# Performance work log

Hardware: AMD Instinct MI355X
Metric: run time of the kernel (lower is better)

Reference implementation:

```python
import jax, jax.numpy as jnp
import numpy as np

B, SX, SY, D = 64, 512, 512, 1024


def setup_inputs() -> dict:
    key = jax.random.key(0)
    k1, k2, k3, k4 = jax.random.split(key, 4)
    x = jax.random.normal(k1, (B, SX, D), dtype=jnp.float32)
    y = jax.random.normal(k2, (B, SY, D), dtype=jnp.float32)
    # Keras 'uniform' init ~ U(-0.05, 0.05); scale kept small and realistic
    W = jax.random.uniform(k3, (D, D), dtype=jnp.float32, minval=-0.05, maxval=0.05)
    b = jax.random.uniform(k4, (D,), dtype=jnp.float32, minval=-0.05, maxval=0.05)
    return {"x": x, "y": y, "W": W, "b": b}


def reference(x, y, W, b):
    # proj: (x @ W + b) -> [B, Sx, D]
    proj = jnp.einsum('bsd,de->bse', x, W) + b
    # attention scores: proj @ y^T -> [B, Sx, Sy]
    att = jnp.einsum('bsd,btd->bst', proj, y)
    # row-wise stable softmax over last axis (matches manual max-subtract softmax)
    nor = jax.nn.softmax(att, axis=-1)
    # weighted sum over y -> [B, Sx, D]
    return jnp.einsum('bst,btd->bsd', nor, y)
```

## Files before the change

### kernel.cpp

```cpp
#include <hip/hip_runtime.h>


typedef float  f32x4  __attribute__((ext_vector_type(4)));
typedef _Float16 f16x8 __attribute__((ext_vector_type(8)));
typedef _Float16 f16x4 __attribute__((ext_vector_type(4)));
typedef __bf16 bf16x8 __attribute__((ext_vector_type(8)));
typedef __bf16 bf16x4 __attribute__((ext_vector_type(4)));

#define MFMA_F16(a, b, c)  __builtin_amdgcn_mfma_f32_16x16x32_f16((a), (b), (c), 0, 0, 0)
#define MFMA_BF16(a, b, c) __builtin_amdgcn_mfma_f32_16x16x32_bf16((a), (b), (c), 0, 0, 0)

#define WAIT_VM(N)  do { asm volatile("s_waitcnt vmcnt(" #N ")" ::: "memory"); \
                         __builtin_amdgcn_sched_barrier(0); } while (0)

__device__ __forceinline__ void async16(const void* g, void* lds) {
    __builtin_amdgcn_global_load_lds(
        (const __attribute__((address_space(1))) unsigned int*)g,
        (__attribute__((address_space(3))) unsigned int*)lds, 16, 0, 0);
}

template <bool DOW>
__global__ void prep_all_kernel(const float* __restrict__ y, _Float16* __restrict__ yf,
                                _Float16* __restrict__ yT, const float* __restrict__ x,
                                f16x4* __restrict__ xh, f16x4* __restrict__ xl,
                                const float* __restrict__ W, _Float16* __restrict__ WT)
{
    __shared__ _Float16 LT[64][72];
    const int tid = threadIdx.x;
    const int bid = blockIdx.x;

    if (bid < 8192) {
        const int b   = bid >> 7;
        const int rem = bid & 127;
        const int sy0 = (rem >> 4) * 64;
        const int d0  = (rem & 15) * 64;
        const int r0 = tid >> 4;
        const int c4 = (tid & 15) * 4;
        #pragma unroll
        for (int i = 0; i < 4; ++i) {
            const int r = r0 + i * 16;
            const float4 v = *(const float4*)&y[((size_t)b * 512 + sy0 + r) * 1024 + d0 + c4];
            const f16x4 hv = {(_Float16)v.x, (_Float16)v.y, (_Float16)v.z, (_Float16)v.w};
            *(f16x4*)&yf[((size_t)b * 512 + sy0 + r) * 1024 + d0 + c4] = hv;
            #pragma unroll
            for (int cc = 0; cc < 4; ++cc) {
                const int c = (cc + (tid & 3)) & 3;
                LT[c4 + c][r] = hv[c];
            }
        }
        __syncthreads();
        #pragma unroll
        for (int i = 0; i < 4; ++i) {
            const int dr = r0 + i * 16;
            const f16x4 v = *(const f16x4*)&LT[dr][(tid & 15) * 4];
            *(f16x4*)&yT[((size_t)b * 1024 + d0 + dr) * 512 + sy0 + (tid & 15) * 4] = v;
        }
    } else if (bid < 10240) {
        int i = (bid - 8192) * 256 + tid;
        const float4* in = (const float4*)x;
        for (; i < 8388608; i += 2048 * 256) {
            const float4 v = in[i];
            const _Float16 h0 = (_Float16)v.x, h1 = (_Float16)v.y,
                           h2 = (_Float16)v.z, h3 = (_Float16)v.w;
            xh[i] = (f16x4){h0, h1, h2, h3};
            xl[i] = (f16x4){(_Float16)(v.x - (float)h0), (_Float16)(v.y - (float)h1),
                            (_Float16)(v.z - (float)h2), (_Float16)(v.w - (float)h3)};
        }
    } else if constexpr (DOW) {
        const int rem = bid - 10240;
        const int k0 = (rem >> 4) * 64;
        const int n0 = (rem & 15) * 64;
        const int r0 = tid >> 4;
        const int c4 = (tid & 15) * 4;
        #pragma unroll
        for (int i = 0; i < 4; ++i) {
            const int r = r0 + i * 16;
            const float4 v = *(const float4*)&W[(size_t)(k0 + r) * 1024 + n0 + c4];
            const f16x4 hv = {(_Float16)v.x, (_Float16)v.y, (_Float16)v.z, (_Float16)v.w};
            #pragma unroll
            for (int cc = 0; cc < 4; ++cc) {
                const int c = (cc + (tid & 3)) & 3;
                LT[c4 + c][r] = hv[c];
            }
        }
        __syncthreads();
        #pragma unroll
        for (int i = 0; i < 4; ++i) {
            const int dr = r0 + i * 16;
            const f16x4 v = *(const f16x4*)&LT[dr][(tid & 15) * 4];
            *(f16x4*)&WT[(size_t)(n0 + dr) * 1024 + k0 + (tid & 15) * 4] = v;
        }
    }
}

template <bool PRE>
__global__ __launch_bounds__(256, 2)
void proj_f16_kernel(const _Float16* __restrict__ xh, const _Float16* __restrict__ xl,
                     const _Float16* __restrict__ WT, const float* __restrict__ W,
                     const float* __restrict__ bias, char* __restrict__ outc)
{
    __shared__ __align__(16) char psm[73728];

    const int tid = threadIdx.x, lane = tid & 63, wave = tid >> 6;
    const int swz = (blockIdx.x & 7) * 256 + (blockIdx.x >> 3);
    const int m0 = (swz >> 3) * 128, n0 = (swz & 7) * 128;
    const int wm = (wave >> 1) * 64, wn = (wave & 1) * 64;
    const int ar = lane & 15;
    const int qs  = ((lane >> 4) ^ ((lane >> 1) & 3)) * 8;
    const int gcS = ((lane & 3) ^ ((lane >> 3) & 3)) * 8;
    const int lrow = lane >> 2;
    const int wkb = tid & 7;
    const int wn4 = (tid >> 3) * 4;

    f32x4 acc[4][4];
    #pragma unroll
    for (int i = 0; i < 4; ++i)
        #pragma unroll
        for (int j = 0; j < 4; ++j)
            acc[i][j] = (f32x4){0.f, 0.f, 0.f, 0.f};

    auto STAGE = [&](int t, int bi) {
        const int k0 = t * 32;
        _Float16 (*Xh)[32] = (_Float16(*)[32])(psm + bi * 24576);
        _Float16 (*Xl)[32] = (_Float16(*)[32])(psm + bi * 24576 + 8192);
        _Float16 (*Wf)[32] = (_Float16(*)[32])(psm + bi * 24576 + 16384);
        #pragma unroll
        for (int tt = 0; tt < 2; ++tt) {
            const int r = wave * 32 + tt * 16 + lrow;
            async16(&xh[(size_t)(m0 + r) * 1024 + k0 + gcS], &Xh[wave * 32 + tt * 16][0]);
            async16(&xl[(size_t)(m0 + r) * 1024 + k0 + gcS], &Xl[wave * 32 + tt * 16][0]);
            if constexpr (PRE)
                async16(&WT[(size_t)(n0 + r) * 1024 + k0 + gcS], &Wf[wave * 32 + tt * 16][0]);
        }
        if constexpr (!PRE) {
            const size_t wb = (size_t)(k0 + wkb * 4) * 1024 + n0 + wn4;
            const float4 v0 = *(const float4*)&W[wb];
            const float4 v1 = *(const float4*)&W[wb + 1024];
            const float4 v2 = *(const float4*)&W[wb + 2048];
            const float4 v3 = *(const float4*)&W[wb + 3072];
            const float rv[4][4] = {{v0.x, v0.y, v0.z, v0.w},
                                    {v1.x, v1.y, v1.z, v1.w},
                                    {v2.x, v2.y, v2.z, v2.w},
                                    {v3.x, v3.y, v3.z, v3.w}};
            #pragma unroll
            for (int j = 0; j < 4; ++j) {
                const int R = wn4 + j;
                const f16x4 hv = {(_Float16)rv[0][j], (_Float16)rv[1][j],
                                  (_Float16)rv[2][j], (_Float16)rv[3][j]};
                const int c = (wkb >> 1) ^ ((R >> 1) & 3);
                *(f16x4*)&Wf[R][c * 8 + (wkb & 1) * 4] = hv;
            }
        }
    };

    STAGE(0, 0);
    STAGE(1, 1);
    STAGE(2, 2);

    int bi = 0;
    for (int t = 0; t < 32; ++t) {
        if (t < 30)       { if constexpr (PRE) WAIT_VM(12); else WAIT_VM(8); }
        else if (t == 30) { if constexpr (PRE) WAIT_VM(6);  else WAIT_VM(4); }
        else              { WAIT_VM(0); }
        __builtin_amdgcn_s_barrier();

        _Float16 (*Xh)[32] = (_Float16(*)[32])(psm + bi * 24576);
        _Float16 (*Xl)[32] = (_Float16(*)[32])(psm + bi * 24576 + 8192);
        _Float16 (*Wf)[32] = (_Float16(*)[32])(psm + bi * 24576 + 16384);
        f16x8 ah[4], al[4], bfv[4];
        #pragma unroll
        for (int f = 0; f < 4; ++f) {
            ah[f]  = *(const f16x8*)&Xh[wm + f * 16 + ar][qs];
            al[f]  = *(const f16x8*)&Xl[wm + f * 16 + ar][qs];
            bfv[f] = *(const f16x8*)&Wf[wn + f * 16 + ar][qs];
        }
        #pragma unroll
        for (int i = 0; i < 4; ++i)
            #pragma unroll
            for (int j = 0; j < 4; ++j) {
                acc[i][j] = MFMA_F16(ah[i], bfv[j], acc[i][j]);
                acc[i][j] = MFMA_F16(al[i], bfv[j], acc[i][j]);
            }
        __builtin_amdgcn_s_barrier();

        if (t < 29) {
            STAGE(t + 3, bi);
            if constexpr (!PRE)
                asm volatile("s_waitcnt lgkmcnt(0)" ::: "memory");
        }
        bi = (bi == 2) ? 0 : bi + 1;
    }

    _Float16* Ep = (_Float16*)psm;
    const int q4 = (lane >> 4) * 4;
    #pragma unroll
    for (int j = 0; j < 4; ++j) {
        const int nloc = wn + j * 16 + ar;
        const float bv = bias[n0 + nloc];
        const int nidx = (nloc >> 3) * 16 + (nloc & 7);
        #pragma unroll
        for (int i = 0; i < 4; ++i)
            #pragma unroll
            for (int r = 0; r < 4; ++r) {
                const int Rl = wm + i * 16 + q4 + r;
                const float v = acc[i][j][r] + bv;
                const _Float16 h = (_Float16)v;
                Ep[Rl * 256 + nidx]     = h;
                Ep[Rl * 256 + nidx + 8] = (_Float16)(v - (float)h);
            }
    }
    __syncthreads();
    #pragma unroll
    for (int c = 0; c < 16; ++c) {
        const int lin = c * 4096 + tid * 16;
        const int row = lin >> 9;
        const int off = lin & 511;
        *(float4*)(outc + (size_t)(m0 + row) * 4096 + n0 * 4 + off)
            = *(const float4*)(psm + lin);
    }
}

__global__ __launch_bounds__(256, 2)
void attn_f16_kernel(const _Float16* __restrict__ yf, const _Float16* __restrict__ yT,
                     char* __restrict__ outc)
{
    __shared__ _Float16 Pbuf[64][520];
    __shared__ float    Red[512];

    const int tid = threadIdx.x, lane = tid & 63, wave = tid >> 6;
    const int swzb = (blockIdx.x & 7) * 64 + (blockIdx.x >> 3);
    const int b = swzb >> 3, sx0 = (swzb & 7) * 64;
    const int pbase = b * 512 + sx0;
    const int ar = lane & 15, q = lane >> 4, qk = q * 8;
    const size_t ybase = (size_t)b * 512 * 1024;

    f32x4 s2[4][8];
    #pragma unroll
    for (int ri = 0; ri < 4; ++ri)
        #pragma unroll
        for (int t = 0; t < 8; ++t)
            s2[ri][t] = (f32x4){0.f, 0.f, 0.f, 0.f};

    const char* aptr = outc + (size_t)(pbase + ar) * 4096;
    const _Float16* yw = yf + ybase + (size_t)(wave * 128 + ar) * 1024;

    f16x8 A0H[4], A0L[4], A1H[4], A1L[4];
    auto LOADA = [&](int kk, f16x8 (&AH)[4], f16x8 (&AL)[4]) {
        #pragma unroll
        for (int ri = 0; ri < 4; ++ri) {
            const char* p = aptr + (size_t)ri * 65536 + (size_t)(kk * 4 + q) * 32;
            AH[ri] = *(const f16x8*)p;
            AL[ri] = *(const f16x8*)(p + 16);
        }
    };

    LOADA(0, A0H, A0L);
    LOADA(1, A1H, A1L);

    for (int kk = 0; kk < 32; kk += 2) {
        {
            f16x8 bf[8];
            #pragma unroll
            for (int t = 0; t < 8; ++t)
                bf[t] = *(const f16x8*)&yw[(size_t)t * 16384 + kk * 32 + qk];
            #pragma unroll
            for (int ri = 0; ri < 4; ++ri)
                #pragma unroll
                for (int t = 0; t < 8; ++t) {
                    s2[ri][t] = MFMA_F16(A0H[ri], bf[t], s2[ri][t]);
                    s2[ri][t] = MFMA_F16(A0L[ri], bf[t], s2[ri][t]);
                }
            if (kk + 2 < 32) LOADA(kk + 2, A0H, A0L);
        }
        {
            f16x8 bf[8];
            #pragma unroll
            for (int t = 0; t < 8; ++t)
                bf[t] = *(const f16x8*)&yw[(size_t)t * 16384 + (kk + 1) * 32 + qk];
            #pragma unroll
            for (int ri = 0; ri < 4; ++ri)
                #pragma unroll
                for (int t = 0; t < 8; ++t) {
                    s2[ri][t] = MFMA_F16(A1H[ri], bf[t], s2[ri][t]);
                    s2[ri][t] = MFMA_F16(A1L[ri], bf[t], s2[ri][t]);
                }
            if (kk + 3 < 32) LOADA(kk + 3, A1H, A1L);
        }
    }

    float pm[4][4];
    #pragma unroll
    for (int ri = 0; ri < 4; ++ri)
        #pragma unroll
        for (int r = 0; r < 4; ++r) {
            float m = -3.0e38f;
            #pragma unroll
            for (int t = 0; t < 8; ++t) m = fmaxf(m, s2[ri][t][r]);
            pm[ri][r] = m;
        }
    #pragma unroll
    for (int off = 1; off < 16; off <<= 1)
        #pragma unroll
        for (int ri = 0; ri < 4; ++ri)
            #pragma unroll
            for (int r = 0; r < 4; ++r)
                pm[ri][r] = fmaxf(pm[ri][r], __shfl_xor(pm[ri][r], off, 64));
    if (ar == 0) {
        #pragma unroll
        for (int ri = 0; ri < 4; ++ri)
            #pragma unroll
            for (int r = 0; r < 4; ++r)
                Red[wave * 64 + ri * 16 + q * 4 + r] = pm[ri][r];
    }
    __syncthreads();
    float gm[4][4];
    #pragma unroll
    for (int ri = 0; ri < 4; ++ri)
        #pragma unroll
        for (int r = 0; r < 4; ++r) {
            const int row = ri * 16 + q * 4 + r;
            gm[ri][r] = fmaxf(fmaxf(Red[row], Red[64 + row]),
                              fmaxf(Red[128 + row], Red[192 + row]));
        }
    float ps[4][4];
    #pragma unroll
    for (int ri = 0; ri < 4; ++ri)
        #pragma unroll
        for (int r = 0; r < 4; ++r) {
            float sum = 0.f;
            #pragma unroll
            for (int t = 0; t < 8; ++t) {
                const float e = __expf(s2[ri][t][r] - gm[ri][r]);
                s2[ri][t][r] = e;
                sum += e;
            }
            ps[ri][r] = sum;
        }
    #pragma unroll
    for (int off = 1; off < 16; off <<= 1)
        #pragma unroll
        for (int ri = 0; ri < 4; ++ri)
            #pragma unroll
            for (int r = 0; r < 4; ++r)
                ps[ri][r] += __shfl_xor(ps[ri][r], off, 64);
    if (ar == 0) {
        #pragma unroll
        for (int ri = 0; ri < 4; ++ri)
            #pragma unroll
            for (int r = 0; r < 4; ++r)
                Red[256 + wave * 64 + ri * 16 + q * 4 + r] = ps[ri][r];
    }
    __syncthreads();
    float inv[4][4];
    #pragma unroll
    for (int ri = 0; ri < 4; ++ri)
        #pragma unroll
        for (int r = 0; r < 4; ++r) {
            const int row = 256 + ri * 16 + q * 4 + r;
            inv[ri][r] = 1.0f / (Red[row] + Red[64 + row] + Red[128 + row] + Red[192 + row]);
        }
    #pragma unroll
    for (int ri = 0; ri < 4; ++ri)
        #pragma unroll
        for (int t = 0; t < 8; ++t)
            #pragma unroll
            for (int r = 0; r < 4; ++r)
                Pbuf[ri * 16 + q * 4 + r][wave * 128 + t * 16 + ar]
                    = (_Float16)(s2[ri][t][r] * inv[ri][r]);
    __syncthreads();

    float* outF = (float*)outc;
    #pragma unroll
    for (int dc = 0; dc < 2; ++dc) {
        f32x4 o2[4][8];
        #pragma unroll
        for (int ri = 0; ri < 4; ++ri)
            #pragma unroll
            for (int t = 0; t < 8; ++t)
                o2[ri][t] = (f32x4){0.f, 0.f, 0.f, 0.f};

        const _Float16* ytw = yT + ((size_t)b * 1024 + wave * 256 + dc * 128 + ar) * 512;

        for (int kk = 0; kk < 16; ++kk) {
            f16x8 a2[4], b2[8];
            #pragma unroll
            for (int ri = 0; ri < 4; ++ri)
                a2[ri] = *(const f16x8*)&Pbuf[ri * 16 + ar][kk * 32 + qk];
            #pragma unroll
            for (int t = 0; t < 8; ++t)
                b2[t] = *(const f16x8*)&ytw[(size_t)t * 16 * 512 + kk * 32 + qk];
            #pragma unroll
            for (int ri = 0; ri < 4; ++ri)
                #pragma unroll
                for (int t = 0; t < 8; ++t)
                    o2[ri][t] = MFMA_F16(a2[ri], b2[t], o2[ri][t]);
        }
        #pragma unroll
        for (int ri = 0; ri < 4; ++ri)
            #pragma unroll
            for (int t = 0; t < 8; ++t)
                #pragma unroll
                for (int r = 0; r < 4; ++r)
                    outF[(size_t)(pbase + ri * 16 + q * 4 + r) * 1024
                         + wave * 256 + dc * 128 + t * 16 + ar] = o2[ri][t][r];
    }
}


__device__ __forceinline__ void cvt4(const float4 v, bf16x4& h, bf16x4& l) {
    const float f0 = v.x, f1 = v.y, f2 = v.z, f3 = v.w;
    const __bf16 h0 = (__bf16)f0, h1 = (__bf16)f1, h2 = (__bf16)f2, h3 = (__bf16)f3;
    h = (bf16x4){h0, h1, h2, h3};
    l = (bf16x4){(__bf16)(f0 - (float)h0), (__bf16)(f1 - (float)h1),
                 (__bf16)(f2 - (float)h2), (__bf16)(f3 - (float)h3)};
}

__global__ __launch_bounds__(256, 2)
void proj_kernel_fb(const float* __restrict__ x, const float* __restrict__ W,
                    const float* __restrict__ bias, float* __restrict__ proj)
{
    __shared__ __bf16 Ah[128][40];
    __shared__ __bf16 Al[128][40];
    __shared__ __bf16 Bh[128][40];
    __shared__ __bf16 Bl[128][40];

    const int tid = threadIdx.x, lane = tid & 63, wave = tid >> 6;
    const int wm = (wave >> 1) * 64, wn = (wave & 1) * 64;
    const int m0 = (blockIdx.x >> 3) * 128, n0 = (blockIdx.x & 7) * 128;
    const int ar = lane & 15, ak = (lane >> 4) * 8;

    f32x4 acc[4][4];
    #pragma unroll
    for (int i = 0; i < 4; ++i)
        #pragma unroll
        for (int j = 0; j < 4; ++j)
            acc[i][j] = (f32x4){0.f, 0.f, 0.f, 0.f};

    const int xr = tid >> 3, xc = (tid & 7) * 4;
    const int wkb = tid >> 5, wn4 = (tid & 31) * 4;

    for (int k0 = 0; k0 < 1024; k0 += 32) {
        __syncthreads();
        #pragma unroll
        for (int it = 0; it < 4; ++it) {
            const int r = xr + it * 32;
            const float4 v = *(const float4*)&x[(size_t)(m0 + r) * 1024 + k0 + xc];
            bf16x4 h, l; cvt4(v, h, l);
            *(bf16x4*)&Ah[r][xc] = h;
            *(bf16x4*)&Al[r][xc] = l;
        }
        {
            const size_t wb = (size_t)(k0 + wkb * 4) * 1024 + n0 + wn4;
            const float4 v0 = *(const float4*)&W[wb];
            const float4 v1 = *(const float4*)&W[wb + 1024];
            const float4 v2 = *(const float4*)&W[wb + 2048];
            const float4 v3 = *(const float4*)&W[wb + 3072];
            const float rv[4][4] = {{v0.x, v0.y, v0.z, v0.w},
                                    {v1.x, v1.y, v1.z, v1.w},
                                    {v2.x, v2.y, v2.z, v2.w},
                                    {v3.x, v3.y, v3.z, v3.w}};
            #pragma unroll
            for (int j = 0; j < 4; ++j) {
                bf16x4 h, l;
                #pragma unroll
                for (int kk = 0; kk < 4; ++kk) {
                    const float f = rv[kk][j];
                    const __bf16 hb = (__bf16)f;
                    h[kk] = hb;
                    l[kk] = (__bf16)(f - (float)hb);
                }
                *(bf16x4*)&Bh[wn4 + j][wkb * 4] = h;
                *(bf16x4*)&Bl[wn4 + j][wkb * 4] = l;
            }
        }
        __syncthreads();

        bf16x8 a_h[4], a_l[4], b_h[4], b_l[4];
        #pragma unroll
        for (int f = 0; f < 4; ++f) {
            a_h[f] = *(const bf16x8*)&Ah[wm + f * 16 + ar][ak];
            a_l[f] = *(const bf16x8*)&Al[wm + f * 16 + ar][ak];
            b_h[f] = *(const bf16x8*)&Bh[wn + f * 16 + ar][ak];
            b_l[f] = *(const bf16x8*)&Bl[wn + f * 16 + ar][ak];
        }
        #pragma unroll
        for (int i = 0; i < 4; ++i)
            #pragma unroll
            for (int j = 0; j < 4; ++j) {
                acc[i][j] = MFMA_BF16(a_h[i], b_h[j], acc[i][j]);
                acc[i][j] = MFMA_BF16(a_l[i], b_h[j], acc[i][j]);
                acc[i][j] = MFMA_BF16(a_h[i], b_l[j], acc[i][j]);
            }
    }

    const int q4 = (lane >> 4) * 4;
    #pragma unroll
    for (int j = 0; j < 4; ++j) {
        const int n = n0 + wn + j * 16 + ar;
        const float bv = bias[n];
        #pragma unroll
        for (int i = 0; i < 4; ++i) {
            const size_t base = (size_t)(m0 + wm + i * 16 + q4) * 1024 + n;
            #pragma unroll
            for (int r = 0; r < 4; ++r)
                proj[base + (size_t)r * 1024] = acc[i][j][r] + bv;
        }
    }
}

__global__ __launch_bounds__(256, 1)
void attn_kernel_fb(const float* __restrict__ y, float* __restrict__ out)
{
    __shared__ __bf16 Ph[64][40];
    __shared__ __bf16 Pl[64][40];
    __shared__ __bf16 Yh[128][40];
    __shared__ __bf16 Yl[128][40];
    __shared__ __bf16 Pbuf[64][520];

    const int tid = threadIdx.x, lane = tid & 63, wave = tid >> 6;
    const int b = blockIdx.x >> 3, sx0 = (blockIdx.x & 7) * 64;
    const size_t ybase = (size_t)b * 512 * 1024;
    const size_t pbase = ((size_t)b * 512 + sx0) * 1024;
    const int ar = lane & 15, ak = (lane >> 4) * 8, q = lane >> 4;

    f32x4 s[4][8];
    #pragma unroll
    for (int nb = 0; nb < 4; ++nb)
        #pragma unroll
        for (int f = 0; f < 8; ++f)
            s[nb][f] = (f32x4){0.f, 0.f, 0.f, 0.f};

    const int pr = tid >> 3, pc = (tid & 7) * 4;

    for (int k0 = 0; k0 < 1024; k0 += 32) {
        __syncthreads();
        #pragma unroll
        for (int it = 0; it < 2; ++it) {
            const int r = pr + it * 32;
            const float4 v = *(const float4*)&out[pbase + (size_t)r * 1024 + k0 + pc];
            bf16x4 h, l; cvt4(v, h, l);
            *(bf16x4*)&Ph[r][pc] = h;
            *(bf16x4*)&Pl[r][pc] = l;
        }
        #pragma unroll
        for (int nb = 0; nb < 4; ++nb) {
            if (nb) __syncthreads();
            const int sy0 = nb * 128;
            #pragma unroll
            for (int it = 0; it < 4; ++it) {
                const int r = pr + it * 32;
                const float4 v = *(const float4*)&y[ybase + (size_t)(sy0 + r) * 1024 + k0 + pc];
                bf16x4 h, l; cvt4(v, h, l);
                *(bf16x4*)&Yh[r][pc] = h;
                *(bf16x4*)&Yl[r][pc] = l;
            }
            __syncthreads();
            const bf16x8 a_h = *(const bf16x8*)&Ph[wave * 16 + ar][ak];
            const bf16x8 a_l = *(const bf16x8*)&Pl[wave * 16 + ar][ak];
            #pragma unroll
            for (int f = 0; f < 8; ++f) {
                const bf16x8 b_h = *(const bf16x8*)&Yh[f * 16 + ar][ak];
                const bf16x8 b_l = *(const bf16x8*)&Yl[f * 16 + ar][ak];
                s[nb][f] = MFMA_BF16(a_h, b_h, s[nb][f]);
                s[nb][f] = MFMA_BF16(a_l, b_h, s[nb][f]);
                s[nb][f] = MFMA_BF16(a_h, b_l, s[nb][f]);
            }
        }
    }

    #pragma unroll
    for (int r = 0; r < 4; ++r) {
        float m = -3.0e38f;
        #pragma unroll
        for (int nb = 0; nb < 4; ++nb)
            #pragma unroll
            for (int f = 0; f < 8; ++f)
                m = fmaxf(m, s[nb][f][r]);
        #pragma unroll
        for (int off = 1; off < 16; off <<= 1)
            m = fmaxf(m, __shfl_xor(m, off, 64));
        float sum = 0.f;
        #pragma unroll
        for (int nb = 0; nb < 4; ++nb)
            #pragma unroll
            for (int f = 0; f < 8; ++f) {
                const float e = __expf(s[nb][f][r] - m);
                s[nb][f][r] = e;
                sum += e;
            }
        #pragma unroll
        for (int off = 1; off < 16; off <<= 1)
            sum += __shfl_xor(sum, off, 64);
        const float inv = 1.0f / sum;
        #pragma unroll
        for (int nb = 0; nb < 4; ++nb)
            #pragma unroll
            for (int f = 0; f < 8; ++f)
                s[nb][f][r] *= inv;
    }
    #pragma unroll
    for (int nb = 0; nb < 4; ++nb)
        #pragma unroll
        for (int f = 0; f < 8; ++f)
            #pragma unroll
            for (int r = 0; r < 4; ++r)
                Pbuf[wave * 16 + q * 4 + r][nb * 128 + f * 16 + ar] = (__bf16)s[nb][f][r];

    const int y2kb = tid >> 5, y2n4 = (tid & 31) * 4;
    for (int d0 = 0; d0 < 1024; d0 += 128) {
        f32x4 o[8];
        #pragma unroll
        for (int f = 0; f < 8; ++f) o[f] = (f32x4){0.f, 0.f, 0.f, 0.f};

        for (int k0 = 0; k0 < 512; k0 += 32) {
            __syncthreads();
            const size_t yb = ybase + (size_t)(k0 + y2kb * 4) * 1024 + d0 + y2n4;
            const float4 v0 = *(const float4*)&y[yb];
            const float4 v1 = *(const float4*)&y[yb + 1024];
            const float4 v2 = *(const float4*)&y[yb + 2048];
            const float4 v3 = *(const float4*)&y[yb + 3072];
            const float rv[4][4] = {{v0.x, v0.y, v0.z, v0.w},
                                    {v1.x, v1.y, v1.z, v1.w},
                                    {v2.x, v2.y, v2.z, v2.w},
                                    {v3.x, v3.y, v3.z, v3.w}};
            #pragma unroll
            for (int j = 0; j < 4; ++j) {
                const bf16x4 h = (bf16x4){(__bf16)rv[0][j], (__bf16)rv[1][j],
                                          (__bf16)rv[2][j], (__bf16)rv[3][j]};
                *(bf16x4*)&Yh[y2n4 + j][y2kb * 4] = h;
            }
            __syncthreads();
            const bf16x8 a = *(const bf16x8*)&Pbuf[wave * 16 + ar][k0 + ak];
            #pragma unroll
            for (int f = 0; f < 8; ++f) {
                const bf16x8 bb = *(const bf16x8*)&Yh[f * 16 + ar][ak];
                o[f] = MFMA_BF16(a, bb, o[f]);
            }
        }
        #pragma unroll
        for (int f = 0; f < 8; ++f)
            #pragma unroll
            for (int r = 0; r < 4; ++r)
                out[pbase + (size_t)(wave * 16 + q * 4 + r) * 1024 + d0 + f * 16 + ar] = o[f][r];
    }
}


extern "C" void kernel_launch(void* const* d_in, const int* in_sizes, int n_in,
                              void* d_out, int out_size, void* d_ws, size_t ws_size,
                              hipStream_t stream) {
    (void)in_sizes; (void)n_in; (void)out_size;
    const float* x    = (const float*)d_in[0];
    const float* y    = (const float*)d_in[1];
    const float* W    = (const float*)d_in[2];
    const float* bias = (const float*)d_in[3];

    if (ws_size >= 268435456ULL) {
        _Float16* yf = (_Float16*)d_ws;
        _Float16* yT = yf + 33554432;
        _Float16* xh = yT + 33554432;
        _Float16* xl = xh + 33554432;
        _Float16* WT = xl + 33554432;
        const bool pre = ws_size >= 268435456ULL + 2097152ULL;

        if (pre) {
            prep_all_kernel<true><<<dim3(10496), dim3(256), 0, stream>>>(
                y, yf, yT, x, (f16x4*)xh, (f16x4*)xl, W, WT);
            proj_f16_kernel<true><<<dim3(2048), dim3(256), 0, stream>>>(xh, xl, WT, W, bias,
                                                                        (char*)d_out);
        } else {
            prep_all_kernel<false><<<dim3(10240), dim3(256), 0, stream>>>(
                y, yf, yT, x, (f16x4*)xh, (f16x4*)xl, W, nullptr);
            proj_f16_kernel<false><<<dim3(2048), dim3(256), 0, stream>>>(xh, xl, nullptr, W,
                                                                         bias, (char*)d_out);
        }
        attn_f16_kernel<<<dim3(512), dim3(256), 0, stream>>>(yf, yT, (char*)d_out);
    } else {
        float* out = (float*)d_out;
        proj_kernel_fb<<<dim3(256 * 8), dim3(256), 0, stream>>>(x, W, bias, out);
        attn_kernel_fb<<<dim3(64 * 8), dim3(256), 0, stream>>>(y, out);
    }
}
```

Before: 693.3 us.

## Stage y tiles through swizzled LDS with async loads in score GEMM

The first GEMM of the attention kernel used to read y fragments straight from global memory into registers. It now double-buffers y K-slices into LDS with global_load_lds async copies, using an XOR swizzle to avoid bank conflicts, and reuses the LDS region that later holds Pbuf. The MFMA order is also split so all high-part products issue before the low-part products. The aim is to overlap y fetches with MFMA work and cut global load latency, at the cost of manual vmcnt accounting. Each wave reads only its own rows, so no barrier is used, which could be a correctness risk.

```diff
diff --git a/kernel.cpp b/kernel.cpp
--- a/kernel.cpp
+++ b/kernel.cpp
@@ -224,14 +224,20 @@
 void attn_f16_kernel(const _Float16* __restrict__ yf, const _Float16* __restrict__ yT,
                      char* __restrict__ outc)
 {
-    __shared__ _Float16 Pbuf[64][520];
-    __shared__ float    Red[512];
+    __shared__ __align__(16) char smem[68608];
+    _Float16 (*Yb0)[32]   = (_Float16(*)[32])smem;
+    _Float16 (*Yb1)[32]   = (_Float16(*)[32])(smem + 32768);
+    _Float16 (*Pbuf)[520] = (_Float16(*)[520])smem;
+    float*    Red         = (float*)(smem + 66560);
 
     const int tid = threadIdx.x, lane = tid & 63, wave = tid >> 6;
     const int swzb = (blockIdx.x & 7) * 64 + (blockIdx.x >> 3);
     const int b = swzb >> 3, sx0 = (swzb & 7) * 64;
     const int pbase = b * 512 + sx0;
     const int ar = lane & 15, q = lane >> 4, qk = q * 8;
+    const int qs  = (q ^ ((lane >> 1) & 3)) * 8;
+    const int gcS = ((lane & 3) ^ ((lane >> 3) & 3)) * 8;
+    const int lrow = lane >> 2;
     const size_t ybase = (size_t)b * 512 * 1024;
 
     f32x4 s2[4][8];
@@ -242,8 +248,15 @@
             s2[ri][t] = (f32x4){0.f, 0.f, 0.f, 0.f};
 
     const char* aptr = outc + (size_t)(pbase + ar) * 4096;
-    const _Float16* yw = yf + ybase + (size_t)(wave * 128 + ar) * 1024;
-
+
+    auto STAGE0 = [&](int kk, _Float16 (*Yb)[32]) {
+        const int k0 = kk * 32;
+        #pragma unroll
+        for (int t = 0; t < 8; ++t) {
+            const int r = wave * 128 + t * 16 + lrow;
+            async16(&yf[ybase + (size_t)r * 1024 + k0 + gcS], &Yb[wave * 128 + t * 16][0]);
+        }
+    };
     f16x8 A0H[4], A0L[4], A1H[4], A1L[4];
     auto LOADA = [&](int kk, f16x8 (&AH)[4], f16x8 (&AL)[4]) {
         #pragma unroll
@@ -253,40 +266,42 @@
             AL[ri] = *(const f16x8*)(p + 16);
         }
     };
-
+    auto HALF = [&](int kk, f16x8 (&AH)[4], f16x8 (&AL)[4], _Float16 (*Yb)[32], bool more) {
+        f16x8 bf[8];
+        #pragma unroll
+        for (int t = 0; t < 8; ++t)
+            bf[t] = *(const f16x8*)&Yb[wave * 128 + t * 16 + ar][qs];
+        #pragma unroll
+        for (int ri = 0; ri < 4; ++ri)
+            #pragma unroll
+            for (int t = 0; t < 8; ++t)
+                s2[ri][t] = MFMA_F16(AH[ri], bf[t], s2[ri][t]);
+        #pragma unroll
+        for (int ri = 0; ri < 4; ++ri)
+            #pragma unroll
+            for (int t = 0; t < 8; ++t)
+                s2[ri][t] = MFMA_F16(AL[ri], bf[t], s2[ri][t]);
+        if (more) {
+            LOADA(kk + 2, AH, AL);
+            STAGE0(kk + 2, Yb);
+        }
+    };
+
+    STAGE0(0, Yb0);
     LOADA(0, A0H, A0L);
     LOADA(1, A1H, A1L);
-
-    for (int kk = 0; kk < 32; kk += 2) {
-        {
-            f16x8 bf[8];
-            #pragma unroll
-            for (int t = 0; t < 8; ++t)
-                bf[t] = *(const f16x8*)&yw[(size_t)t * 16384 + kk * 32 + qk];
-            #pragma unroll
-            for (int ri = 0; ri < 4; ++ri)
-                #pragma unroll
-                for (int t = 0; t < 8; ++t) {
-                    s2[ri][t] = MFMA_F16(A0H[ri], bf[t], s2[ri][t]);
-                    s2[ri][t] = MFMA_F16(A0L[ri], bf[t], s2[ri][t]);
-                }
-            if (kk + 2 < 32) LOADA(kk + 2, A0H, A0L);
-        }
-        {
-            f16x8 bf[8];
-            #pragma unroll
-            for (int t = 0; t < 8; ++t)
-                bf[t] = *(const f16x8*)&yw[(size_t)t * 16384 + (kk + 1) * 32 + qk];
-            #pragma unroll
-            for (int ri = 0; ri < 4; ++ri)
-                #pragma unroll
-                for (int t = 0; t < 8; ++t) {
-                    s2[ri][t] = MFMA_F16(A1H[ri], bf[t], s2[ri][t]);
-                    s2[ri][t] = MFMA_F16(A1L[ri], bf[t], s2[ri][t]);
-                }
-            if (kk + 3 < 32) LOADA(kk + 3, A1H, A1L);
-        }
-    }
+    STAGE0(1, Yb1);
+
+    for (int kk = 0; kk < 30; kk += 2) {
+        WAIT_VM(16);
+        HALF(kk, A0H, A0L, Yb0, true);
+        WAIT_VM(16);
+        HALF(kk + 1, A1H, A1L, Yb1, true);
+    }
+    WAIT_VM(16);
+    HALF(30, A0H, A0L, Yb0, false);
+    WAIT_VM(0);
+    HALF(31, A1H, A1L, Yb1, false);
 
     float pm[4][4];
     #pragma unroll
```

New measurement: 739.2 us. 1.07x slower.

## Split score computation into two column halves with online-softmax rescaling

Applied to the files above, without the earlier changes.

The attention kernel now computes the 64x512 score tile in two passes of 256 columns each. Each wave holds a 4x4 accumulator block instead of 4x8, which cuts register pressure. The B operand is now register double-buffered alongside A. Softmax is done flash-style: each half is exponentiated against its own running max, the first half in LDS is rescaled by exp(m1-m), and the 1/sum normalization is deferred to the output store. The cost is an extra pass over the first half of Pbuf, more reductions and barriers, and re-reading the A operand twice.

```diff
diff --git a/kernel.cpp b/kernel.cpp
--- a/kernel.cpp
+++ b/kernel.cpp
@@ -225,7 +225,7 @@
                      char* __restrict__ outc)
 {
     __shared__ _Float16 Pbuf[64][520];
-    __shared__ float    Red[512];
+    __shared__ float    Red[1024];
 
     const int tid = threadIdx.x, lane = tid & 63, wave = tid >> 6;
     const int swzb = (blockIdx.x & 7) * 64 + (blockIdx.x >> 3);
@@ -234,15 +234,7 @@
     const int ar = lane & 15, q = lane >> 4, qk = q * 8;
     const size_t ybase = (size_t)b * 512 * 1024;
 
-    f32x4 s2[4][8];
-    #pragma unroll
-    for (int ri = 0; ri < 4; ++ri)
-        #pragma unroll
-        for (int t = 0; t < 8; ++t)
-            s2[ri][t] = (f32x4){0.f, 0.f, 0.f, 0.f};
-
     const char* aptr = outc + (size_t)(pbase + ar) * 4096;
-    const _Float16* yw = yf + ybase + (size_t)(wave * 128 + ar) * 1024;
 
     f16x8 A0H[4], A0L[4], A1H[4], A1L[4];
     auto LOADA = [&](int kk, f16x8 (&AH)[4], f16x8 (&AL)[4]) {
@@ -253,120 +245,254 @@
             AL[ri] = *(const f16x8*)(p + 16);
         }
     };
-
-    LOADA(0, A0H, A0L);
-    LOADA(1, A1H, A1L);
-
-    for (int kk = 0; kk < 32; kk += 2) {
-        {
-            f16x8 bf[8];
-            #pragma unroll
-            for (int t = 0; t < 8; ++t)
-                bf[t] = *(const f16x8*)&yw[(size_t)t * 16384 + kk * 32 + qk];
-            #pragma unroll
-            for (int ri = 0; ri < 4; ++ri)
-                #pragma unroll
-                for (int t = 0; t < 8; ++t) {
-                    s2[ri][t] = MFMA_F16(A0H[ri], bf[t], s2[ri][t]);
-                    s2[ri][t] = MFMA_F16(A0L[ri], bf[t], s2[ri][t]);
+    f16x8 B0[4], B1[4];
+    auto LOADB = [&](int cb, int kk, f16x8 (&Bv)[4]) {
+        #pragma unroll
+        for (int t = 0; t < 4; ++t)
+            Bv[t] = *(const f16x8*)&yf[ybase + (size_t)(cb + t * 16 + ar) * 1024
+                                       + kk * 32 + qk];
+    };
+
+    f32x4 s2[4][4];
+    float mp1[4][4];
+    float inv_[4][4];
+
+    {
+        const int cb = wave * 64;
+        #pragma unroll
+        for (int ri = 0; ri < 4; ++ri)
+            #pragma unroll
+            for (int t = 0; t < 4; ++t)
+                s2[ri][t] = (f32x4){0.f, 0.f, 0.f, 0.f};
+        LOADA(0, A0H, A0L);
+        LOADA(1, A1H, A1L);
+        LOADB(cb, 0, B0);
+        LOADB(cb, 1, B1);
+        for (int kk = 0; kk < 32; kk += 2) {
+            #pragma unroll
+            for (int ri = 0; ri < 4; ++ri)
+                #pragma unroll
+                for (int t = 0; t < 4; ++t) {
+                    s2[ri][t] = MFMA_F16(A0H[ri], B0[t], s2[ri][t]);
+                    s2[ri][t] = MFMA_F16(A0L[ri], B0[t], s2[ri][t]);
                 }
-            if (kk + 2 < 32) LOADA(kk + 2, A0H, A0L);
-        }
-        {
-            f16x8 bf[8];
-            #pragma unroll
-            for (int t = 0; t < 8; ++t)
-                bf[t] = *(const f16x8*)&yw[(size_t)t * 16384 + (kk + 1) * 32 + qk];
-            #pragma unroll
-            for (int ri = 0; ri < 4; ++ri)
-                #pragma unroll
-                for (int t = 0; t < 8; ++t) {
-                    s2[ri][t] = MFMA_F16(A1H[ri], bf[t], s2[ri][t]);
-                    s2[ri][t] = MFMA_F16(A1L[ri], bf[t], s2[ri][t]);
+            if (kk + 2 < 32) { LOADA(kk + 2, A0H, A0L); LOADB(cb, kk + 2, B0); }
+            #pragma unroll
+            for (int ri = 0; ri < 4; ++ri)
+                #pragma unroll
+                for (int t = 0; t < 4; ++t) {
+                    s2[ri][t] = MFMA_F16(A1H[ri], B1[t], s2[ri][t]);
+                    s2[ri][t] = MFMA_F16(A1L[ri], B1[t], s2[ri][t]);
                 }
-            if (kk + 3 < 32) LOADA(kk + 3, A1H, A1L);
-        }
-    }
-
-    float pm[4][4];
-    #pragma unroll
-    for (int ri = 0; ri < 4; ++ri)
-        #pragma unroll
-        for (int r = 0; r < 4; ++r) {
-            float m = -3.0e38f;
-            #pragma unroll
-            for (int t = 0; t < 8; ++t) m = fmaxf(m, s2[ri][t][r]);
-            pm[ri][r] = m;
-        }
-    #pragma unroll
-    for (int off = 1; off < 16; off <<= 1)
-        #pragma unroll
-        for (int ri = 0; ri < 4; ++ri)
-            #pragma unroll
-            for (int r = 0; r < 4; ++r)
-                pm[ri][r] = fmaxf(pm[ri][r], __shfl_xor(pm[ri][r], off, 64));
-    if (ar == 0) {
-        #pragma unroll
-        for (int ri = 0; ri < 4; ++ri)
-            #pragma unroll
-            for (int r = 0; r < 4; ++r)
-                Red[wave * 64 + ri * 16 + q * 4 + r] = pm[ri][r];
-    }
-    __syncthreads();
-    float gm[4][4];
+            if (kk + 3 < 32) { LOADA(kk + 3, A1H, A1L); LOADB(cb, kk + 3, B1); }
+        }
+        float pm[4][4];
+        #pragma unroll
+        for (int ri = 0; ri < 4; ++ri)
+            #pragma unroll
+            for (int r = 0; r < 4; ++r) {
+                float m = -3.0e38f;
+                #pragma unroll
+                for (int t = 0; t < 4; ++t) m = fmaxf(m, s2[ri][t][r]);
+                pm[ri][r] = m;
+            }
+        #pragma unroll
+        for (int off = 1; off < 16; off <<= 1)
+            #pragma unroll
+            for (int ri = 0; ri < 4; ++ri)
+                #pragma unroll
+                for (int r = 0; r < 4; ++r)
+                    pm[ri][r] = fmaxf(pm[ri][r], __shfl_xor(pm[ri][r], off, 64));
+        if (ar == 0) {
+            #pragma unroll
+            for (int ri = 0; ri < 4; ++ri)
+                #pragma unroll
+                for (int r = 0; r < 4; ++r)
+                    Red[wave * 64 + ri * 16 + q * 4 + r] = pm[ri][r];
+        }
+        __syncthreads();
+        #pragma unroll
+        for (int ri = 0; ri < 4; ++ri)
+            #pragma unroll
+            for (int r = 0; r < 4; ++r) {
+                const int row = ri * 16 + q * 4 + r;
+                mp1[ri][r] = fmaxf(fmaxf(Red[row], Red[64 + row]),
+                                   fmaxf(Red[128 + row], Red[192 + row]));
+            }
+        if (wave == 0 && ar == 0) {
+            #pragma unroll
+            for (int ri = 0; ri < 4; ++ri)
+                #pragma unroll
+                for (int r = 0; r < 4; ++r)
+                    Red[512 + ri * 16 + q * 4 + r] = mp1[ri][r];
+        }
+        float ps[4][4];
+        #pragma unroll
+        for (int ri = 0; ri < 4; ++ri)
+            #pragma unroll
+            for (int r = 0; r < 4; ++r) {
+                float sum = 0.f;
+                #pragma unroll
+                for (int t = 0; t < 4; ++t) {
+                    const float e = __expf(s2[ri][t][r] - mp1[ri][r]);
+                    s2[ri][t][r] = e;
+                    sum += e;
+                }
+                ps[ri][r] = sum;
+            }
+        #pragma unroll
+        for (int off = 1; off < 16; off <<= 1)
+            #pragma unroll
+            for (int ri = 0; ri < 4; ++ri)
+                #pragma unroll
+                for (int r = 0; r < 4; ++r)
+                    ps[ri][r] += __shfl_xor(ps[ri][r], off, 64);
+        if (ar == 0) {
+            #pragma unroll
+            for (int ri = 0; ri < 4; ++ri)
+                #pragma unroll
+                for (int r = 0; r < 4; ++r)
+                    Red[256 + wave * 64 + ri * 16 + q * 4 + r] = ps[ri][r];
+        }
+        #pragma unroll
+        for (int ri = 0; ri < 4; ++ri)
+            #pragma unroll
+            for (int t = 0; t < 4; ++t)
+                #pragma unroll
+                for (int r = 0; r < 4; ++r)
+                    Pbuf[ri * 16 + q * 4 + r][cb + t * 16 + ar]
+                        = (_Float16)s2[ri][t][r];
+        __syncthreads();
+    }
+
+    {
+        const int cb = 256 + wave * 64;
+        #pragma unroll
+        for (int ri = 0; ri < 4; ++ri)
+            #pragma unroll
+            for (int t = 0; t < 4; ++t)
+                s2[ri][t] = (f32x4){0.f, 0.f, 0.f, 0.f};
+        LOADA(0, A0H, A0L);
+        LOADA(1, A1H, A1L);
+        LOADB(cb, 0, B0);
+        LOADB(cb, 1, B1);
+        for (int kk = 0; kk < 32; kk += 2) {
+            #pragma unroll
+            for (int ri = 0; ri < 4; ++ri)
+                #pragma unroll
+                for (int t = 0; t < 4; ++t) {
+                    s2[ri][t] = MFMA_F16(A0H[ri], B0[t], s2[ri][t]);
+                    s2[ri][t] = MFMA_F16(A0L[ri], B0[t], s2[ri][t]);
+                }
+            if (kk + 2 < 32) { LOADA(kk + 2, A0H, A0L); LOADB(cb, kk + 2, B0); }
+            #pragma unroll
+            for (int ri = 0; ri < 4; ++ri)
+                #pragma unroll
+                for (int t = 0; t < 4; ++t) {
+                    s2[ri][t] = MFMA_F16(A1H[ri], B1[t], s2[ri][t]);
+                    s2[ri][t] = MFMA_F16(A1L[ri], B1[t], s2[ri][t]);
+                }
+            if (kk + 3 < 32) { LOADA(kk + 3, A1H, A1L); LOADB(cb, kk + 3, B1); }
+        }
+        float pm[4][4];
+        #pragma unroll
+        for (int ri = 0; ri < 4; ++ri)
+            #pragma unroll
+            for (int r = 0; r < 4; ++r) {
+                float m = -3.0e38f;
+                #pragma unroll
+                for (int t = 0; t < 4; ++t) m = fmaxf(m, s2[ri][t][r]);
+                pm[ri][r] = m;
+            }
+        #pragma unroll
+        for (int off = 1; off < 16; off <<= 1)
+            #pragma unroll
+            for (int ri = 0; ri < 4; ++ri)
+                #pragma unroll
+                for (int r = 0; r < 4; ++r)
+                    pm[ri][r] = fmaxf(pm[ri][r], __shfl_xor(pm[ri][r], off, 64));
+        if (ar == 0) {
+            #pragma unroll
+            for (int ri = 0; ri < 4; ++ri)
+                #pragma unroll
+                for (int r = 0; r < 4; ++r)
+                    Red[wave * 64 + ri * 16 + q * 4 + r] = pm[ri][r];
+        }
+        __syncthreads();
+        float ps[4][4];
+        #pragma unroll
+        for (int ri = 0; ri < 4; ++ri)
+            #pragma unroll
+            for (int r = 0; r < 4; ++r) {
+                const int row = ri * 16 + q * 4 + r;
+                const float m2 = fmaxf(fmaxf(Red[row], Red[64 + row]),
+                                       fmaxf(Red[128 + row], Red[192 + row]));
+                const float m = fmaxf(mp1[ri][r], m2);
+                float sum = 0.f;
+                #pragma unroll
+                for (int t = 0; t < 4; ++t) {
+                    const float e = __expf(s2[ri][t][r] - m);
+                    s2[ri][t][r] = e;
+                    sum += e;
+                }
+                ps[ri][r] = sum;
+            }
+        #pragma unroll
+        for (int off = 1; off < 16; off <<= 1)
+            #pragma unroll
+            for (int ri = 0; ri < 4; ++ri)
+                #pragma unroll
+                for (int r = 0; r < 4; ++r)
+                    ps[ri][r] += __shfl_xor(ps[ri][r], off, 64);
+        if (ar == 0) {
+            #pragma unroll
+            for (int ri = 0; ri < 4; ++ri)
+                #pragma unroll
+                for (int r = 0; r < 4; ++r)
+                    Red[576 + wave * 64 + ri * 16 + q * 4 + r] = ps[ri][r];
+        }
+        #pragma unroll
+        for (int ri = 0; ri < 4; ++ri)
+            #pragma unroll
+            for (int t = 0; t < 4; ++t)
+                #pragma unroll
+                for (int r = 0; r < 4; ++r)
+                    Pbuf[ri * 16 + q * 4 + r][cb + t * 16 + ar]
+                        = (_Float16)s2[ri][t][r];
+        __syncthreads();
+    }
+
+    {
+        const int srow = tid >> 2;
+        const int c0 = (tid & 3) * 64;
+        const float m1r = Red[512 + srow];
+        const float m2r = fmaxf(fmaxf(Red[srow], Red[64 + srow]),
+                                fmaxf(Red[128 + srow], Red[192 + srow]));
+        const float a1 = __expf(m1r - fmaxf(m1r, m2r));
+        #pragma unroll
+        for (int cs = 0; cs < 8; ++cs) {
+            f16x8 v = *(f16x8*)&Pbuf[srow][c0 + cs * 8];
+            #pragma unroll
+            for (int e = 0; e < 8; ++e)
+                v[e] = (_Float16)((float)v[e] * a1);
+            *(f16x8*)&Pbuf[srow][c0 + cs * 8] = v;
+        }
+    }
     #pragma unroll
     for (int ri = 0; ri < 4; ++ri)
         #pragma unroll
         for (int r = 0; r < 4; ++r) {
             const int row = ri * 16 + q * 4 + r;
-            gm[ri][r] = fmaxf(fmaxf(Red[row], Red[64 + row]),
-                              fmaxf(Red[128 + row], Red[192 + row]));
-        }
-    float ps[4][4];
-    #pragma unroll
-    for (int ri = 0; ri < 4; ++ri)
-        #pragma unroll
-        for (int r = 0; r < 4; ++r) {
-            float sum = 0.f;
-            #pragma unroll
-            for (int t = 0; t < 8; ++t) {
-                const float e = __expf(s2[ri][t][r] - gm[ri][r]);
-                s2[ri][t][r] = e;
-                sum += e;
-            }
-            ps[ri][r] = sum;
-        }
-    #pragma unroll
-    for (int off = 1; off < 16; off <<= 1)
-        #pragma unroll
-        for (int ri = 0; ri < 4; ++ri)
-            #pragma unroll
-            for (int r = 0; r < 4; ++r)
-                ps[ri][r] += __shfl_xor(ps[ri][r], off, 64);
-    if (ar == 0) {
-        #pragma unroll
-        for (int ri = 0; ri < 4; ++ri)
-            #pragma unroll
-            for (int r = 0; r < 4; ++r)
-                Red[256 + wave * 64 + ri * 16 + q * 4 + r] = ps[ri][r];
-    }
-    __syncthreads();
-    float inv[4][4];
-    #pragma unroll
-    for (int ri = 0; ri < 4; ++ri)
-        #pragma unroll
-        for (int r = 0; r < 4; ++r) {
-            const int row = 256 + ri * 16 + q * 4 + r;
-            inv[ri][r] = 1.0f / (Red[row] + Red[64 + row] + Red[128 + row] + Red[192 + row]);
-        }
-    #pragma unroll
-    for (int ri = 0; ri < 4; ++ri)
-        #pragma unroll
-        for (int t = 0; t < 8; ++t)
-            #pragma unroll
-            for (int r = 0; r < 4; ++r)
-                Pbuf[ri * 16 + q * 4 + r][wave * 128 + t * 16 + ar]
-                    = (_Float16)(s2[ri][t][r] * inv[ri][r]);
+            const float m1r = Red[512 + row];
+            const float m2r = fmaxf(fmaxf(Red[row], Red[64 + row]),
+                                    fmaxf(Red[128 + row], Red[192 + row]));
+            const float a1 = __expf(m1r - fmaxf(m1r, m2r));
+            const float s1 = Red[256 + row] + Red[320 + row] + Red[384 + row]
+                           + Red[448 + row];
+            const float s2v = Red[576 + row] + Red[640 + row] + Red[704 + row]
+                            + Red[768 + row];
+            inv_[ri][r] = 1.0f / (a1 * s1 + s2v);
+        }
     __syncthreads();
 
     float* outF = (float*)outc;
@@ -402,7 +528,8 @@
                 #pragma unroll
                 for (int r = 0; r < 4; ++r)
                     outF[(size_t)(pbase + ri * 16 + q * 4 + r) * 1024
-                         + wave * 256 + dc * 128 + t * 16 + ar] = o2[ri][t][r];
+                         + wave * 256 + dc * 128 + t * 16 + ar]
+                        = o2[ri][t][r] * inv_[ri][r];
     }
 }
 
```

After: 744.5 us. 7.4% more time.

## Stage y tiles through swizzled LDS via async global-to-LDS loads in attention kernel

Applied to the files above, without the earlier changes.

The attention kernel's score GEMM now brings y tiles into a swizzled LDS staging buffer with global_load_lds async copies. It prefetches the next k-slice while the MFMAs run, where before each wave loaded B fragments directly from global memory into registers. The PV GEMM is restructured into 8 d-chunks, each wave taking 32 columns with yT staged through LDS the same way. This cuts register pressure. The staging buffer aliases the Pbuf region. The tiny single-slice buffers and full vmcnt(0) waits each iteration leave little real overlap, so latency may become exposed.

```diff
diff --git a/kernel.cpp b/kernel.cpp
--- a/kernel.cpp
+++ b/kernel.cpp
@@ -12,6 +12,8 @@
 
 #define WAIT_VM(N)  do { asm volatile("s_waitcnt vmcnt(" #N ")" ::: "memory"); \
                          __builtin_amdgcn_sched_barrier(0); } while (0)
+#define WAIT_LGKM0() do { asm volatile("s_waitcnt lgkmcnt(0)" ::: "memory"); \
+                          __builtin_amdgcn_sched_barrier(0); } while (0)
 
 __device__ __forceinline__ void async16(const void* g, void* lds) {
     __builtin_amdgcn_global_load_lds(
@@ -224,14 +226,20 @@
 void attn_f16_kernel(const _Float16* __restrict__ yf, const _Float16* __restrict__ yT,
                      char* __restrict__ outc)
 {
-    __shared__ _Float16 Pbuf[64][520];
-    __shared__ float    Red[512];
+    __shared__ __align__(16) char smem[76800];
+    _Float16 (*Yst)[32]   = (_Float16(*)[32])smem;
+    _Float16 (*Pbuf)[520] = (_Float16(*)[520])smem;
+    _Float16 (*Yt)[32]    = (_Float16(*)[32])(smem + 66560);
+    float*    Red         = (float*)(smem + 74752);
 
     const int tid = threadIdx.x, lane = tid & 63, wave = tid >> 6;
     const int swzb = (blockIdx.x & 7) * 64 + (blockIdx.x >> 3);
     const int b = swzb >> 3, sx0 = (swzb & 7) * 64;
     const int pbase = b * 512 + sx0;
     const int ar = lane & 15, q = lane >> 4, qk = q * 8;
+    const int qs  = (q ^ ((lane >> 1) & 3)) * 8;
+    const int gcS = ((lane & 3) ^ ((lane >> 3) & 3)) * 8;
+    const int lrow = lane >> 2;
     const size_t ybase = (size_t)b * 512 * 1024;
 
     f32x4 s2[4][8];
@@ -242,49 +250,51 @@
             s2[ri][t] = (f32x4){0.f, 0.f, 0.f, 0.f};
 
     const char* aptr = outc + (size_t)(pbase + ar) * 4096;
-    const _Float16* yw = yf + ybase + (size_t)(wave * 128 + ar) * 1024;
-
-    f16x8 A0H[4], A0L[4], A1H[4], A1L[4];
-    auto LOADA = [&](int kk, f16x8 (&AH)[4], f16x8 (&AL)[4]) {
-        #pragma unroll
-        for (int ri = 0; ri < 4; ++ri) {
-            const char* p = aptr + (size_t)ri * 65536 + (size_t)(kk * 4 + q) * 32;
-            AH[ri] = *(const f16x8*)p;
-            AL[ri] = *(const f16x8*)(p + 16);
-        }
-    };
-
-    LOADA(0, A0H, A0L);
-    LOADA(1, A1H, A1L);
-
-    for (int kk = 0; kk < 32; kk += 2) {
-        {
-            f16x8 bf[8];
-            #pragma unroll
-            for (int t = 0; t < 8; ++t)
-                bf[t] = *(const f16x8*)&yw[(size_t)t * 16384 + kk * 32 + qk];
-            #pragma unroll
-            for (int ri = 0; ri < 4; ++ri)
-                #pragma unroll
-                for (int t = 0; t < 8; ++t) {
-                    s2[ri][t] = MFMA_F16(A0H[ri], bf[t], s2[ri][t]);
-                    s2[ri][t] = MFMA_F16(A0L[ri], bf[t], s2[ri][t]);
-                }
-            if (kk + 2 < 32) LOADA(kk + 2, A0H, A0L);
-        }
-        {
-            f16x8 bf[8];
-            #pragma unroll
-            for (int t = 0; t < 8; ++t)
-                bf[t] = *(const f16x8*)&yw[(size_t)t * 16384 + (kk + 1) * 32 + qk];
-            #pragma unroll
-            for (int ri = 0; ri < 4; ++ri)
-                #pragma unroll
-                for (int t = 0; t < 8; ++t) {
-                    s2[ri][t] = MFMA_F16(A1H[ri], bf[t], s2[ri][t]);
-                    s2[ri][t] = MFMA_F16(A1L[ri], bf[t], s2[ri][t]);
-                }
-            if (kk + 3 < 32) LOADA(kk + 3, A1H, A1L);
+
+    #pragma unroll
+    for (int t = 0; t < 8; ++t) {
+        const int r = wave * 128 + t * 16 + lrow;
+        async16(&yf[ybase + (size_t)r * 1024 + gcS], &Yst[wave * 128 + t * 16][0]);
+    }
+    f16x8 aH[4], aL[4];
+    #pragma unroll
+    for (int ri = 0; ri < 4; ++ri) {
+        const char* p = aptr + (size_t)ri * 65536 + (size_t)q * 32;
+        aH[ri] = *(const f16x8*)p;
+        aL[ri] = *(const f16x8*)(p + 16);
+    }
+
+    for (int kk = 0; kk < 32; ++kk) {
+        WAIT_VM(0);
+        f16x8 bf0[8];
+        #pragma unroll
+        for (int t = 0; t < 8; ++t)
+            bf0[t] = *(const f16x8*)&Yst[wave * 128 + t * 16 + ar][qs];
+        WAIT_LGKM0();
+        if (kk < 31) {
+            const int k1 = (kk + 1) * 32;
+            #pragma unroll
+            for (int t = 0; t < 8; ++t) {
+                const int r = wave * 128 + t * 16 + lrow;
+                async16(&yf[ybase + (size_t)r * 1024 + k1 + gcS],
+                        &Yst[wave * 128 + t * 16][0]);
+            }
+        }
+        #pragma unroll
+        for (int ri = 0; ri < 4; ++ri)
+            #pragma unroll
+            for (int t = 0; t < 8; ++t) {
+                s2[ri][t] = MFMA_F16(aH[ri], bf0[t], s2[ri][t]);
+                s2[ri][t] = MFMA_F16(aL[ri], bf0[t], s2[ri][t]);
+            }
+        if (kk < 31) {
+            #pragma unroll
+            for (int ri = 0; ri < 4; ++ri) {
+                const char* p = aptr + (size_t)ri * 65536
+                              + (size_t)((kk + 1) * 4 + q) * 32;
+                aH[ri] = *(const f16x8*)p;
+                aL[ri] = *(const f16x8*)(p + 16);
+            }
         }
     }
 
@@ -370,39 +380,54 @@
     __syncthreads();
 
     float* outF = (float*)outc;
-    #pragma unroll
-    for (int dc = 0; dc < 2; ++dc) {
-        f32x4 o2[4][8];
+    for (int dc = 0; dc < 8; ++dc) {
+        f32x4 o2[4][2];
         #pragma unroll
         for (int ri = 0; ri < 4; ++ri)
             #pragma unroll
-            for (int t = 0; t < 8; ++t)
+            for (int t = 0; t < 2; ++t)
                 o2[ri][t] = (f32x4){0.f, 0.f, 0.f, 0.f};
 
-        const _Float16* ytw = yT + ((size_t)b * 1024 + wave * 256 + dc * 128 + ar) * 512;
-
+        WAIT_LGKM0();
+        #pragma unroll
+        for (int t = 0; t < 2; ++t) {
+            const int r = wave * 32 + t * 16 + lrow;
+            async16(&yT[(size_t)(b * 1024 + dc * 128 + r) * 512 + gcS],
+                    &Yt[wave * 32 + t * 16][0]);
+        }
         for (int kk = 0; kk < 16; ++kk) {
-            f16x8 a2[4], b2[8];
+            WAIT_VM(0);
+            f16x8 a2[4], b2[2];
             #pragma unroll
             for (int ri = 0; ri < 4; ++ri)
                 a2[ri] = *(const f16x8*)&Pbuf[ri * 16 + ar][kk * 32 + qk];
             #pragma unroll
-            for (int t = 0; t < 8; ++t)
-                b2[t] = *(const f16x8*)&ytw[(size_t)t * 16 * 512 + kk * 32 + qk];
+            for (int t = 0; t < 2; ++t)
+                b2[t] = *(const f16x8*)&Yt[wave * 32 + t * 16 + ar][qs];
+            WAIT_LGKM0();
+            if (kk < 15) {
+                const int k1 = (kk + 1) * 32;
+                #pragma unroll
+                for (int t = 0; t < 2; ++t) {
+                    const int r = wave * 32 + t * 16 + lrow;
+                    async16(&yT[(size_t)(b * 1024 + dc * 128 + r) * 512 + k1 + gcS],
+                            &Yt[wave * 32 + t * 16][0]);
+                }
+            }
             #pragma unroll
             for (int ri = 0; ri < 4; ++ri)
                 #pragma unroll
-                for (int t = 0; t < 8; ++t)
+                for (int t = 0; t < 2; ++t)
                     o2[ri][t] = MFMA_F16(a2[ri], b2[t], o2[ri][t]);
         }
         #pragma unroll
         for (int ri = 0; ri < 4; ++ri)
             #pragma unroll
-            for (int t = 0; t < 8; ++t)
+            for (int t = 0; t < 2; ++t)
                 #pragma unroll
                 for (int r = 0; r < 4; ++r)
                     outF[(size_t)(pbase + ri * 16 + q * 4 + r) * 1024
-                         + wave * 256 + dc * 128 + t * 16 + ar] = o2[ri][t][r];
+                         + dc * 128 + wave * 32 + t * 16 + ar] = o2[ri][t][r];
     }
 }
 
```

After: 689.0 us. No clear change (-0.6%).
